# Kernel tuning notes

Hardware: AMD Instinct MI355X
Metric: run time of the kernel (lower is better)

The kernel has to match this reference:

```python
import jax, jax.numpy as jnp
import numpy as np

B, N, M, H = 200, 384, 512, 128
NN = B * N  # total nodes across the batch of graphs


def _gcn_layer(h, src, dst, norm, W, b):
    # GCNConv: linear -> symmetric-normalized aggregation -> relu
    h = h @ W + b
    msg = h[src] * norm[:, None]
    agg = jax.ops.segment_sum(msg, dst, num_segments=NN)
    return jax.nn.relu(agg)


def setup_inputs() -> dict:
    key = jax.random.key(0)
    ks = jax.random.split(key, 16)
    x = jax.random.normal(ks[0], (NN, 2), dtype=jnp.float32)
    off = (jnp.arange(B) * N)[:, None]
    parent = jax.random.randint(ks[1], (B, M), 0, N) + off
    child = jax.random.randint(ks[2], (B, M), 0, N) + off
    row0 = jnp.concatenate([parent, child], axis=1).reshape(-1)
    row1 = jnp.concatenate([child, parent], axis=1).reshape(-1)
    edge_index = jnp.stack([row0, row1]).astype(jnp.int64)
    numSwitches = jax.random.randint(ks[3], (B,), 1, M // 4).astype(jnp.int64)
    inv_degree = jax.random.uniform(ks[4], (B, N), minval=0.5, maxval=1.5)
    inc_parents = jax.random.normal(ks[5], (B, N, M)) * 0.1
    inc_childs = jax.random.normal(ks[6], (B, N, M)) * 0.1
    A = jax.random.normal(ks[7], (N, M)) * 0.1
    s = lambda k, sh: jax.random.normal(k, sh) * (1.0 / np.sqrt(sh[0]))
    return dict(
        x=x, edge_index=edge_index, numSwitches=numSwitches,
        inv_degree=inv_degree, inc_parents=inc_parents, inc_childs=inc_childs, A=A,
        W1=s(ks[8], (2, H)), b1=jnp.zeros((H,)),
        W2=s(ks[9], (H, H)), b2=jnp.zeros((H,)),
        Ws1=s(ks[10], (3 * H, 4 * H)), bs1=jnp.zeros((4 * H,)),
        Ws2=s(ks[11], (4 * H, 4)), bs2=jnp.zeros((4,)),
        Wc1=s(ks[12], (3 * H, 3 * H)), bc1=jnp.zeros((3 * H,)),
        Wc2=s(ks[13], (3 * H, 3)), bc2=jnp.zeros((3,)),
    )


def reference(x, inv_degree, inc_parents, inc_childs, A,
              W1, b1, W2, b2, Ws1, bs1, Ws2, bs2, Wc1, bc1, Wc2, bc2,
              edge_index, numSwitches):
    # ---- 2-layer GCN with self loops + symmetric norm ----
    src, dst = edge_index[0], edge_index[1]
    loop = jnp.arange(NN)
    src2 = jnp.concatenate([src, loop])
    dst2 = jnp.concatenate([dst, loop])
    deg = jax.ops.segment_sum(jnp.ones_like(src2, dtype=x.dtype), dst2, num_segments=NN)
    dinv = jax.lax.rsqrt(deg)
    norm = dinv[src2] * dinv[dst2]
    h = _gcn_layer(x, src2, dst2, norm, W1, b1)
    xg = _gcn_layer(h, src2, dst2, norm, W2, b2)  # [NN, H]

    x_nn = xg.reshape(B, N, H)
    x_g = x_nn.sum(axis=1)  # graph-level readout [B, H]

    edges = edge_index[0].reshape(B, 2 * M)
    parent_e = edges[:, :M]  # [B, M] global node ids
    child_e = edges[:, M:]
    # last numSwitches[b] edges of graph b are switches
    mask = jnp.arange(M)[None, :] >= (M - numSwitches[:, None])  # [B, M]

    xp = xg[parent_e]  # [B, M, H]
    xc = xg[child_e]
    feat = jnp.concatenate(
        [xp, xc, jnp.broadcast_to(x_g[:, None, :], (B, M, H))], axis=-1)  # [B,M,3H]
    # compute both MLPs densely, then mask-select (same values at selected slots
    # as torch's boolean gather -> MLP -> scatter)
    smlp = jax.nn.relu(feat @ Ws1 + bs1) @ Ws2 + bs2  # [B, M, 4]
    cmlp = jax.nn.relu(feat @ Wc1 + bc1) @ Wc2 + bc2  # [B, M, 3]

    p_switch = jax.nn.sigmoid(smlp[..., 0])
    graph_topo = jnp.where(mask, p_switch, 1.0)
    ps_flow = jnp.where(mask, smlp[..., 1], 0.0)
    vs_parent = jnp.where(mask, smlp[..., 2], 0.0)
    vs_child = jnp.where(mask, smlp[..., 3], 0.0)
    pc_flow = jnp.where(mask, 0.0, cmlp[..., 0])
    vc_parent = jnp.where(mask, 0.0, cmlp[..., 1])
    vc_child = jnp.where(mask, 0.0, cmlp[..., 2])
    p_flow = ps_flow + pc_flow

    # D_inv @ inc @ v is a per-row diagonal scale; no need to build [B,N,N]
    v = inv_degree * (jnp.einsum('bnm,bm->bn', inc_parents, vc_parent + vs_parent)
                      + jnp.einsum('bnm,bm->bn', inc_childs, vc_child + vs_child))
    v = v.at[:, 0].set(1.0)  # slack bus voltage

    # ---- complete_JA (physics completion) ----
    x_input = x.reshape(B, N, 2)
    pl, ql = x_input[..., 0], x_input[..., 1]
    p_fc = p_flow * graph_topo
    q_fc = jnp.einsum('nm,bn->bm', A, v) * graph_topo
    pg = pl + jnp.einsum('nm,bm->bn', A, p_fc)
    qg = ql + jnp.einsum('nm,bm->bn', A, q_fc)

    z = jnp.concatenate([p_fc, v, graph_topo], axis=1)    # [B, M+N+M]
    zc = jnp.concatenate([q_fc, pg, qg], axis=1)          # [B, M+N+N]
    return (z, zc)
```

## Files before the change

kernel.cpp:

```cpp
#include <hip/hip_runtime.h>
#include <hip/hip_bf16.h>

typedef __hip_bfloat16 bf16;
typedef __bf16 bf16x8 __attribute__((ext_vector_type(8)));
typedef float f32x4 __attribute__((ext_vector_type(4)));

static constexpr int cB = 200, cN = 384, cM = 512, cH = 128;
static constexpr int cNN  = cB * cN;
static constexpr int cE   = 2 * cB * cM;
static constexpr int cTWOM = 2 * cM;
static constexpr int ZROW = 2 * cM + cN;
static constexpr int CROW = cM + 2 * cN;
static constexpr int ZBASE = cB * ZROW;

__device__ __forceinline__ float b2f(bf16 x) { return __bfloat162float(x); }
__device__ __forceinline__ bf16  f2b(float x) { return __float2bfloat16(x); }

struct bf2 { bf16 x, y; };

__global__ __launch_bounds__(256) void k_norm_idx(const int* __restrict__ ei_raw,
                                                  const int* __restrict__ nsw_raw,
                                                  int* __restrict__ ei, int* __restrict__ nsw) {
  int z = 0;
#pragma unroll
  for (int j = 1; j < 64; j += 2) z |= ei_raw[j];
  const int f = (z == 0) ? 1 : 0;
  const int i = blockIdx.x * 256 + threadIdx.x;
  if (i < 2 * cE) ei[i] = ei_raw[i << f];
  if (blockIdx.x == 0 && threadIdx.x < cB) nsw[threadIdx.x] = nsw_raw[threadIdx.x << f];
}

__global__ __launch_bounds__(512) void k_csr2(const int* __restrict__ ei,
                                              float* __restrict__ dinv_g,
                                              int* __restrict__ csr_off, int* __restrict__ csr_src,
                                              float* __restrict__ csr_nrm) {
  __shared__ int cnt[cN];
  __shared__ float sdinv[cN];
  __shared__ int base[cN];
  __shared__ int scanbuf[cN];
  const int tid = threadIdx.x;
  const int b = blockIdx.x;
  for (int i = tid; i < cN; i += 512) cnt[i] = 0;
  __syncthreads();
  for (int i = tid; i < cTWOM; i += 512) {
    const int d = ei[cE + b * cTWOM + i] - b * cN;
    atomicAdd(&cnt[d], 1);
  }
  __syncthreads();
  if (tid < cN) {
    const float dv = rsqrtf((float)cnt[tid] + 1.0f);
    sdinv[tid] = dv;
    dinv_g[b * cN + tid] = dv;
    scanbuf[tid] = cnt[tid];
  }
  __syncthreads();
  for (int off = 1; off < cN; off <<= 1) {
    int v = 0;
    if (tid < cN && tid >= off) v = scanbuf[tid - off];
    __syncthreads();
    if (tid < cN) scanbuf[tid] += v;
    __syncthreads();
  }
  if (tid < cN) {
    base[tid] = scanbuf[tid] - cnt[tid];
    csr_off[b * (cN + 1) + tid] = base[tid];
  }
  if (tid == 0) csr_off[b * (cN + 1) + cN] = scanbuf[cN - 1];
  if (tid < cN) cnt[tid] = 0;
  __syncthreads();
  for (int i = tid; i < cTWOM; i += 512) {
    const int e = b * cTWOM + i;
    const int s = ei[e];
    const int d = ei[cE + e];
    const int sl = s - b * cN;
    const int dl = d - b * cN;
    const int slot = base[dl] + atomicAdd(&cnt[dl], 1);
    csr_src[b * cTWOM + slot] = s;
    csr_nrm[b * cTWOM + slot] = sdinv[sl] * sdinv[dl];
  }
}

__global__ __launch_bounds__(384) void k_gath3(const int* __restrict__ csr_off,
                                               const int* __restrict__ csr_src,
                                               const float* __restrict__ csr_nrm,
                                               const float* __restrict__ x,
                                               const float* __restrict__ dinv,
                                               float* __restrict__ a0_w, float* __restrict__ a1_w,
                                               float* __restrict__ aw_w) {
  __shared__ float xs[cN * 2];
  const int b = blockIdx.x, tid = threadIdx.x;
  for (int i = tid; i < cN * 2; i += 384) xs[i] = x[(size_t)b * cN * 2 + i];
  __syncthreads();
  const int nl = tid;
  const int wid = b * cN + nl;
  const int beg = csr_off[b * (cN + 1) + nl];
  const int end = csr_off[b * (cN + 1) + nl + 1];
  const int ebase = b * cTWOM;
  float a0 = 0.f, a1 = 0.f, aw = 0.f;
  for (int j = beg; j < end; ++j) {
    const int sl = csr_src[ebase + j] - b * cN;
    const float w = csr_nrm[ebase + j];
    a0 = fmaf(xs[2 * sl], w, a0);
    a1 = fmaf(xs[2 * sl + 1], w, a1);
    aw += w;
  }
  const float dn = dinv[wid];
  const float dn2 = dn * dn;
  a0 = fmaf(xs[2 * nl], dn2, a0);
  a1 = fmaf(xs[2 * nl + 1], dn2, a1);
  aw += dn2;
  a0_w[wid] = a0;
  a1_w[wid] = a1;
  aw_w[wid] = aw;
}

__global__ __launch_bounds__(256) void k_h1a(const float* __restrict__ a0_w,
                                             const float* __restrict__ a1_w,
                                             const float* __restrict__ aw_w,
                                             const float* __restrict__ W1,
                                             const float* __restrict__ b1,
                                             bf16* __restrict__ h1) {
  const int idx = blockIdx.x * 256 + threadIdx.x;
  if (idx >= cNN * cH) return;
  const int n = idx >> 7, h = idx & 127;
  const float v = a0_w[n] * W1[h] + a1_w[n] * W1[cH + h] + aw_w[n] * b1[h];
  h1[idx] = f2b(fmaxf(v, 0.f));
}

__global__ __launch_bounds__(256) void k_gather(const int* __restrict__ csr_off,
                                                const int* __restrict__ csr_src,
                                                const float* __restrict__ csr_nrm,
                                                const bf16* __restrict__ hsrc,
                                                const float* __restrict__ dinv,
                                                bf16* __restrict__ hdst) {
  const int wid = blockIdx.x * 4 + (threadIdx.x >> 6);
  const int lane = threadIdx.x & 63;
  const int b = wid / cN;
  const int nl = wid - b * cN;
  const int beg = csr_off[b * (cN + 1) + nl];
  const int end = csr_off[b * (cN + 1) + nl + 1];
  const int ebase = b * cTWOM;
  float a0 = 0.f, a1 = 0.f;
  for (int j = beg; j < end; ++j) {
    const int s = csr_src[ebase + j];
    const float w = csr_nrm[ebase + j];
    const unsigned u = *(const unsigned*)(hsrc + (size_t)s * cH + lane * 2);
    a0 = fmaf(__uint_as_float(u << 16), w, a0);
    a1 = fmaf(__uint_as_float(u & 0xffff0000u), w, a1);
  }
  const float dn = dinv[wid];
  const float dn2 = dn * dn;
  const unsigned us = *(const unsigned*)(hsrc + (size_t)wid * cH + lane * 2);
  a0 = fmaf(__uint_as_float(us << 16), dn2, a0);
  a1 = fmaf(__uint_as_float(us & 0xffff0000u), dn2, a1);
  bf2 pk;
  pk.x = f2b(fmaxf(a0, 0.f));
  pk.y = f2b(fmaxf(a1, 0.f));
  *(bf2*)(hdst + (size_t)wid * cH + lane * 2) = pk;
}

__global__ __launch_bounds__(256) void k_lin2_mfma(const bf16* __restrict__ h1,
                                                   const bf16* __restrict__ W2t,
                                                   const float* __restrict__ b2v,
                                                   bf16* __restrict__ h2raw) {
  constexpr int FS = 136;
  __shared__ __align__(16) bf16 feat[64 * FS];
  __shared__ float bl[cH];
  const int tid = threadIdx.x;
  const int n0 = blockIdx.x * 64;
  const int wv = tid >> 6, ln = tid & 63;
  const int fr = ln & 15, g4 = ln >> 4, ak = g4 * 8;
  {
    const int e = tid >> 2, j = tid & 3;
    const uint4* ps = (const uint4*)(h1 + (size_t)(n0 + e) * cH);
    uint4* fp = (uint4*)(feat + e * FS);
#pragma unroll
    for (int r = 0; r < 4; ++r) fp[j * 4 + r] = ps[j * 4 + r];
  }
  for (int i = tid; i < cH; i += 256) bl[i] = b2v[i];
  bf16x8 Bf[2][4];
#pragma unroll
  for (int nt = 0; nt < 2; ++nt) {
    const bf16* bp = W2t + (size_t)(wv * 32 + nt * 16 + fr) * cH + ak;
#pragma unroll
    for (int kt = 0; kt < 4; ++kt) Bf[nt][kt] = *(const bf16x8*)(bp + kt * 32);
  }
  __syncthreads();
#pragma unroll
  for (int mt = 0; mt < 4; ++mt) {
    f32x4 acc0 = f32x4{0.f, 0.f, 0.f, 0.f};
    f32x4 acc1 = f32x4{0.f, 0.f, 0.f, 0.f};
    const bf16* ap = feat + (mt * 16 + fr) * FS + ak;
#pragma unroll
    for (int kt = 0; kt < 4; ++kt) {
      const bf16x8 a = *(const bf16x8*)(ap + kt * 32);
      acc0 = __builtin_amdgcn_mfma_f32_16x16x32_bf16(a, Bf[0][kt], acc0, 0, 0, 0);
      acc1 = __builtin_amdgcn_mfma_f32_16x16x32_bf16(a, Bf[1][kt], acc1, 0, 0, 0);
    }
#pragma unroll
    for (int j = 0; j < 2; ++j) {
      const int col = wv * 32 + j * 16 + fr;
      const f32x4 av = j ? acc1 : acc0;
#pragma unroll
      for (int i = 0; i < 4; ++i) {
        const int row = mt * 16 + g4 * 4 + i;
        h2raw[(size_t)(n0 + row) * cH + col] = f2b(av[i] + bl[col]);
      }
    }
  }
}

__global__ __launch_bounds__(512) void k_xgg(const bf16* __restrict__ xg,
                                             const float* __restrict__ Ws1, const float* __restrict__ bs1,
                                             const float* __restrict__ Wc1, const float* __restrict__ bc1,
                                             float* __restrict__ g_s, float* __restrict__ g_c) {
  __shared__ float red[4][cH];
  __shared__ float xs[cH];
  const int b = blockIdx.x, tid = threadIdx.x;
  {
    const int h = tid & 127, q = tid >> 7;
    float s = 0.f;
    const bf16* p = xg + (size_t)b * cN * cH + (size_t)q * 96 * cH + h;
#pragma unroll 8
    for (int n = 0; n < 96; ++n) s += b2f(p[(size_t)n * cH]);
    red[q][h] = s;
  }
  __syncthreads();
  if (tid < cH) xs[tid] = red[0][tid] + red[1][tid] + red[2][tid] + red[3][tid];
  __syncthreads();
  {
    float acc = bs1[tid];
    for (int k = 0; k < cH; ++k) acc = fmaf(xs[k], Ws1[(2 * cH + k) * 512 + tid], acc);
    g_s[b * 512 + tid] = acc;
  }
  if (tid < 384) {
    float acc = bc1[tid];
    for (int k = 0; k < cH; ++k) acc = fmaf(xs[k], Wc1[(2 * cH + k) * 384 + tid], acc);
    g_c[b * 384 + tid] = acc;
  }
}

__global__ __launch_bounds__(256) void k_wt(const float* __restrict__ Ws1, const float* __restrict__ Wc1,
                                            const float* __restrict__ Wc2, const float* __restrict__ W2,
                                            bf16* __restrict__ Ws1t, bf16* __restrict__ Wc1t,
                                            float* __restrict__ Wc2p, bf16* __restrict__ W2t) {
  int idx = blockIdx.x * 256 + threadIdx.x;
  if (idx < 512 * 256) {
    int j = idx >> 8, k = idx & 255;
    Ws1t[idx] = f2b(Ws1[k * 512 + j]);
  }
  if (idx < 384 * 256) {
    int j = idx >> 8, k = idx & 255;
    Wc1t[idx] = f2b(Wc1[k * 384 + j]);
  }
  if (idx < 128 * 128) {
    int j = idx >> 7, k = idx & 127;
    W2t[idx] = f2b(W2[k * 128 + j]);
  }
  if (idx < 384 * 4) {
    int j = idx >> 2, o = idx & 3;
    Wc2p[idx] = (o < 3) ? Wc2[j * 3 + o] : 0.f;
  }
}

__global__ __launch_bounds__(256) void k_mlp_mfma(
    const int* __restrict__ ei, const int* __restrict__ nsw, const bf16* __restrict__ xg,
    const bf16* __restrict__ Ws1t, const bf16* __restrict__ Wc1t,
    const float* __restrict__ g_s, const float* __restrict__ g_c,
    const float* __restrict__ Ws2, const float* __restrict__ bs2,
    const float* __restrict__ Wc2p, const float* __restrict__ bc2,
    float* __restrict__ gt_w, float* __restrict__ wvp_w, float* __restrict__ wvc_w,
    float* __restrict__ pfc_w, float* __restrict__ out) {
  constexpr int FS = 264;
  __shared__ __align__(16) bf16 feat[64 * FS];
  __shared__ float gsl[512];
  __shared__ float gcl[384];
  __shared__ float red_s[4][64][4];
  __shared__ float red_c[4][64][4];

  const int tid = threadIdx.x;
  const int b = blockIdx.x >> 3;
  const int m0 = (blockIdx.x & 7) << 6;
  const int wv = tid >> 6, ln = tid & 63;
  const int fr = ln & 15;
  const int g4 = ln >> 4;
  const int swz = (fr & 7) * 8;

  const int ns = nsw[b];
  const int mb = cM - ns;
  const bool needS = (m0 + 64 > mb);
  const bool needC = (m0 < mb);

  {
    const int e = tid >> 2, j = tid & 3;
    const int m = m0 + e;
    const int pn = ei[b * cTWOM + m];
    const int cn = ei[b * cTWOM + cM + m];
    const int es = e & 7;
    const uint4* ps = (const uint4*)(xg + (size_t)pn * cH);
    const uint4* cs = (const uint4*)(xg + (size_t)cn * cH);
    uint4* fp = (uint4*)(feat + e * FS);
    uint4* fc = (uint4*)(feat + e * FS + 128);
#pragma unroll
    for (int r = 0; r < 4; ++r) {
      const int i = j * 4 + r;
      fp[i ^ es] = ps[i];
      fc[i ^ es] = cs[i];
    }
  }
  if (needS) for (int i = tid; i < 512; i += 256) gsl[i] = g_s[b * 512 + i];
  if (needC) for (int i = tid; i < 384; i += 256) gcl[i] = g_c[b * 384 + i];
  __syncthreads();

  if (needS) {
    float p[4][4][4];
#pragma unroll
    for (int m = 0; m < 4; ++m)
#pragma unroll
      for (int i = 0; i < 4; ++i)
#pragma unroll
        for (int o = 0; o < 4; ++o) p[m][i][o] = 0.f;
    const bf16* bp = Ws1t + ((size_t)(wv * 128 + fr)) * 256 + g4 * 8;
#pragma unroll
    for (int c = 0; c < 2; ++c) {
      f32x4 acc[4][4];
#pragma unroll
      for (int m = 0; m < 4; ++m)
#pragma unroll
        for (int j = 0; j < 4; ++j) acc[m][j] = f32x4{0.f, 0.f, 0.f, 0.f};
      const bf16* bpc = bp + (size_t)(c * 4) * 16 * 256;
#pragma unroll
      for (int kt = 0; kt < 8; ++kt) {
        const int eo = (g4 * 8 + kt * 32) ^ swz;
        const bf16x8 a0 = *(const bf16x8*)(feat + fr * FS + eo);
        const bf16x8 a1 = *(const bf16x8*)(feat + (16 + fr) * FS + eo);
        const bf16x8 a2 = *(const bf16x8*)(feat + (32 + fr) * FS + eo);
        const bf16x8 a3 = *(const bf16x8*)(feat + (48 + fr) * FS + eo);
        const int ko = kt * 32;
#pragma unroll
        for (int j = 0; j < 4; ++j) {
          const bf16x8 bfr = *(const bf16x8*)(bpc + (size_t)j * 16 * 256 + ko);
          acc[0][j] = __builtin_amdgcn_mfma_f32_16x16x32_bf16(a0, bfr, acc[0][j], 0, 0, 0);
          acc[1][j] = __builtin_amdgcn_mfma_f32_16x16x32_bf16(a1, bfr, acc[1][j], 0, 0, 0);
          acc[2][j] = __builtin_amdgcn_mfma_f32_16x16x32_bf16(a2, bfr, acc[2][j], 0, 0, 0);
          acc[3][j] = __builtin_amdgcn_mfma_f32_16x16x32_bf16(a3, bfr, acc[3][j], 0, 0, 0);
        }
      }
#pragma unroll
      for (int j = 0; j < 4; ++j) {
        const int col = wv * 128 + (c * 4 + j) * 16 + fr;
        const float4 w4 = *(const float4*)(Ws2 + col * 4);
        const float gs = gsl[col];
#pragma unroll
        for (int m = 0; m < 4; ++m)
#pragma unroll
          for (int i = 0; i < 4; ++i) {
            const float hv = fmaxf(acc[m][j][i] + gs, 0.f);
            p[m][i][0] = fmaf(hv, w4.x, p[m][i][0]);
            p[m][i][1] = fmaf(hv, w4.y, p[m][i][1]);
            p[m][i][2] = fmaf(hv, w4.z, p[m][i][2]);
            p[m][i][3] = fmaf(hv, w4.w, p[m][i][3]);
          }
      }
    }
#pragma unroll
    for (int mask = 1; mask <= 8; mask <<= 1)
#pragma unroll
      for (int m = 0; m < 4; ++m)
#pragma unroll
        for (int i = 0; i < 4; ++i)
#pragma unroll
          for (int o = 0; o < 4; ++o) p[m][i][o] += __shfl_xor(p[m][i][o], mask);
    if (fr == 0) {
#pragma unroll
      for (int m = 0; m < 4; ++m)
#pragma unroll
        for (int i = 0; i < 4; ++i) {
          const int row = m * 16 + g4 * 4 + i;
#pragma unroll
          for (int o = 0; o < 4; ++o) red_s[wv][row][o] = p[m][i][o];
        }
    }
  }

  if (needC) {
    float p[4][4][4];
#pragma unroll
    for (int m = 0; m < 4; ++m)
#pragma unroll
      for (int i = 0; i < 4; ++i)
#pragma unroll
        for (int o = 0; o < 4; ++o) p[m][i][o] = 0.f;
    const bf16* bp = Wc1t + ((size_t)(wv * 96 + fr)) * 256 + g4 * 8;
#pragma unroll
    for (int c = 0; c < 2; ++c) {
      f32x4 acc[4][3];
#pragma unroll
      for (int m = 0; m < 4; ++m)
#pragma unroll
        for (int j = 0; j < 3; ++j) acc[m][j] = f32x4{0.f, 0.f, 0.f, 0.f};
      const bf16* bpc = bp + (size_t)(c * 3) * 16 * 256;
#pragma unroll
      for (int kt = 0; kt < 8; ++kt) {
        const int eo = (g4 * 8 + kt * 32) ^ swz;
        const bf16x8 a0 = *(const bf16x8*)(feat + fr * FS + eo);
        const bf16x8 a1 = *(const bf16x8*)(feat + (16 + fr) * FS + eo);
        const bf16x8 a2 = *(const bf16x8*)(feat + (32 + fr) * FS + eo);
        const bf16x8 a3 = *(const bf16x8*)(feat + (48 + fr) * FS + eo);
        const int ko = kt * 32;
#pragma unroll
        for (int j = 0; j < 3; ++j) {
          const bf16x8 bfr = *(const bf16x8*)(bpc + (size_t)j * 16 * 256 + ko);
          acc[0][j] = __builtin_amdgcn_mfma_f32_16x16x32_bf16(a0, bfr, acc[0][j], 0, 0, 0);
          acc[1][j] = __builtin_amdgcn_mfma_f32_16x16x32_bf16(a1, bfr, acc[1][j], 0, 0, 0);
          acc[2][j] = __builtin_amdgcn_mfma_f32_16x16x32_bf16(a2, bfr, acc[2][j], 0, 0, 0);
          acc[3][j] = __builtin_amdgcn_mfma_f32_16x16x32_bf16(a3, bfr, acc[3][j], 0, 0, 0);
        }
      }
#pragma unroll
      for (int j = 0; j < 3; ++j) {
        const int col = wv * 96 + (c * 3 + j) * 16 + fr;
        const float4 w4 = *(const float4*)(Wc2p + col * 4);
        const float gc = gcl[col];
#pragma unroll
        for (int m = 0; m < 4; ++m)
#pragma unroll
          for (int i = 0; i < 4; ++i) {
            const float hv = fmaxf(acc[m][j][i] + gc, 0.f);
            p[m][i][0] = fmaf(hv, w4.x, p[m][i][0]);
            p[m][i][1] = fmaf(hv, w4.y, p[m][i][1]);
            p[m][i][2] = fmaf(hv, w4.z, p[m][i][2]);
          }
      }
    }
#pragma unroll
    for (int mask = 1; mask <= 8; mask <<= 1)
#pragma unroll
      for (int m = 0; m < 4; ++m)
#pragma unroll
        for (int i = 0; i < 4; ++i)
#pragma unroll
          for (int o = 0; o < 3; ++o) p[m][i][o] += __shfl_xor(p[m][i][o], mask);
    if (fr == 0) {
#pragma unroll
      for (int m = 0; m < 4; ++m)
#pragma unroll
        for (int i = 0; i < 4; ++i) {
          const int row = m * 16 + g4 * 4 + i;
#pragma unroll
          for (int o = 0; o < 3; ++o) red_c[wv][row][o] = p[m][i][o];
        }
    }
  }
  __syncthreads();

  if (tid < 64) {
    const int e = tid, m = m0 + e;
    const bool mk = (m >= mb);
    float gt, pf, vp, vc;
    if (mk) {
      const float s0  = red_s[0][e][0] + red_s[1][e][0] + red_s[2][e][0] + red_s[3][e][0] + bs2[0];
      gt = 1.f / (1.f + expf(-s0));
      pf = red_s[0][e][1] + red_s[1][e][1] + red_s[2][e][1] + red_s[3][e][1] + bs2[1];
      vp = red_s[0][e][2] + red_s[1][e][2] + red_s[2][e][2] + red_s[3][e][2] + bs2[2];
      vc = red_s[0][e][3] + red_s[1][e][3] + red_s[2][e][3] + red_s[3][e][3] + bs2[3];
    } else {
      gt = 1.f;
      pf = red_c[0][e][0] + red_c[1][e][0] + red_c[2][e][0] + red_c[3][e][0] + bc2[0];
      vp = red_c[0][e][1] + red_c[1][e][1] + red_c[2][e][1] + red_c[3][e][1] + bc2[1];
      vc = red_c[0][e][2] + red_c[1][e][2] + red_c[2][e][2] + red_c[3][e][2] + bc2[2];
    }
    const float pfc = pf * gt;
    const int bm = b * cM + m;
    gt_w[bm] = gt; wvp_w[bm] = vp; wvc_w[bm] = vc; pfc_w[bm] = pfc;
    out[b * ZROW + m] = pfc;
    out[b * ZROW + cM + cN + m] = gt;
  }
}

__global__ __launch_bounds__(256) void k_v(const float* __restrict__ incP, const float* __restrict__ incC,
                                           const float* __restrict__ wvp, const float* __restrict__ wvc,
                                           const float* __restrict__ invdeg, float* __restrict__ v_w,
                                           float* __restrict__ out) {
  const int wid = blockIdx.x * 4 + (threadIdx.x >> 6);
  const int lane = threadIdx.x & 63;
  const int b = wid / cN, n = wid % cN;
  const size_t rowoff = (size_t)(b * cN + n) * cM + lane * 8;
  const float4 p0 = *(const float4*)(incP + rowoff);
  const float4 p1 = *(const float4*)(incP + rowoff + 4);
  const float4 c0 = *(const float4*)(incC + rowoff);
  const float4 c1 = *(const float4*)(incC + rowoff + 4);
  const float* wp = wvp + b * cM + lane * 8;
  const float* wc = wvc + b * cM + lane * 8;
  float s;
  s = p0.x * wp[0] + p0.y * wp[1] + p0.z * wp[2] + p0.w * wp[3] +
      p1.x * wp[4] + p1.y * wp[5] + p1.z * wp[6] + p1.w * wp[7];
  s += c0.x * wc[0] + c0.y * wc[1] + c0.z * wc[2] + c0.w * wc[3] +
       c1.x * wc[4] + c1.y * wc[5] + c1.z * wc[6] + c1.w * wc[7];
#pragma unroll
  for (int off = 32; off >= 1; off >>= 1) s += __shfl_down(s, off);
  if (lane == 0) {
    float val = invdeg[b * cN + n] * s;
    if (n == 0) val = 1.0f;
    v_w[b * cN + n] = val;
    out[b * ZROW + cM + n] = val;
  }
}

__global__ __launch_bounds__(256) void k_qfc(const float* __restrict__ A, const float* __restrict__ v_w,
                                             const float* __restrict__ gt_w, float* __restrict__ qfc_w,
                                             float* __restrict__ out) {
  __shared__ float vs[cN];
  const int b = blockIdx.x >> 1;
  const int m = ((blockIdx.x & 1) << 8) + threadIdx.x;
  for (int i = threadIdx.x; i < cN; i += 256) vs[i] = v_w[b * cN + i];
  __syncthreads();
  float s = 0.f;
  for (int n = 0; n < cN; ++n) s = fmaf(A[n * cM + m], vs[n], s);
  const int bm = b * cM + m;
  const float q = s * gt_w[bm];
  qfc_w[bm] = q;
  out[ZBASE + b * CROW + m] = q;
}

__global__ __launch_bounds__(256) void k_pgqg(const float* __restrict__ A, const float* __restrict__ x,
                                              const float* __restrict__ pfc, const float* __restrict__ qfc,
                                              float* __restrict__ out) {
  const int wid = blockIdx.x * 4 + (threadIdx.x >> 6);
  const int lane = threadIdx.x & 63;
  const int b = wid / cN, n = wid - b * cN;
  const float* ar = A + (size_t)n * cM + lane * 8;
  const float* pf = pfc + b * cM + lane * 8;
  const float* qf = qfc + b * cM + lane * 8;
  const float4 a0 = *(const float4*)(ar);
  const float4 a1 = *(const float4*)(ar + 4);
  float ps, qs;
  ps = a0.x * pf[0] + a0.y * pf[1] + a0.z * pf[2] + a0.w * pf[3] +
       a1.x * pf[4] + a1.y * pf[5] + a1.z * pf[6] + a1.w * pf[7];
  qs = a0.x * qf[0] + a0.y * qf[1] + a0.z * qf[2] + a0.w * qf[3] +
       a1.x * qf[4] + a1.y * qf[5] + a1.z * qf[6] + a1.w * qf[7];
#pragma unroll
  for (int off = 32; off >= 1; off >>= 1) {
    ps += __shfl_down(ps, off);
    qs += __shfl_down(qs, off);
  }
  if (lane == 0) {
    out[ZBASE + b * CROW + cM + n] = x[2 * (size_t)wid] + ps;
    out[ZBASE + b * CROW + cM + cN + n] = x[2 * (size_t)wid + 1] + qs;
  }
}

extern "C" void kernel_launch(void* const* d_in, const int* in_sizes, int n_in,
                              void* d_out, int out_size, void* d_ws, size_t ws_size,
                              hipStream_t stream) {
  const bool dict_order = (in_sizes[1] == 2 * cE);
  int IEI, INSW, IIVD, IIP, IIC, IA, IW;
  if (dict_order) { IEI = 1; INSW = 2; IIVD = 3; IIP = 4; IIC = 5; IA = 6; IW = 7; }
  else            { IIVD = 1; IIP = 2; IIC = 3; IA = 4; IW = 5; IEI = 17; INSW = 18; }

  const float* x = (const float*)d_in[0];
  const int* ei_raw = (const int*)d_in[IEI];
  const int* nsw_raw = (const int*)d_in[INSW];
  const float* invdeg = (const float*)d_in[IIVD];
  const float* incP = (const float*)d_in[IIP];
  const float* incC = (const float*)d_in[IIC];
  const float* A = (const float*)d_in[IA];
  const float* W1 = (const float*)d_in[IW + 0];
  const float* b1 = (const float*)d_in[IW + 1];
  const float* W2 = (const float*)d_in[IW + 2];
  const float* b2 = (const float*)d_in[IW + 3];
  const float* Ws1 = (const float*)d_in[IW + 4];
  const float* bs1 = (const float*)d_in[IW + 5];
  const float* Ws2 = (const float*)d_in[IW + 6];
  const float* bs2 = (const float*)d_in[IW + 7];
  const float* Wc1 = (const float*)d_in[IW + 8];
  const float* bc1 = (const float*)d_in[IW + 9];
  const float* Wc2 = (const float*)d_in[IW + 10];
  const float* bc2 = (const float*)d_in[IW + 11];
  float* out = (float*)d_out;

  char* w = (char*)d_ws;
  auto alloc = [&](size_t bytes) { void* p = (void*)w; w += (bytes + 255) & ~(size_t)255; return p; };
  float* dinv = (float*)alloc((size_t)cNN * 4);
  int* ei = (int*)alloc((size_t)2 * cE * 4);
  int* nsw = (int*)alloc((size_t)cB * 4);
  bf16* hbufA = (bf16*)alloc((size_t)cNN * cH * 2);
  bf16* hbufB = (bf16*)alloc((size_t)cNN * cH * 2);
  int* csr_off = (int*)alloc((size_t)cB * (cN + 1) * 4);
  int* csr_src = (int*)alloc((size_t)cE * 4);
  float* csr_nrm = (float*)alloc((size_t)cE * 4);
  float* a0_w = (float*)alloc((size_t)cNN * 4);
  float* a1_w = (float*)alloc((size_t)cNN * 4);
  float* aw_w = (float*)alloc((size_t)cNN * 4);
  bf16* Ws1t = (bf16*)alloc((size_t)512 * 256 * 2);
  bf16* Wc1t = (bf16*)alloc((size_t)384 * 256 * 2);
  bf16* W2t = (bf16*)alloc((size_t)128 * 128 * 2);
  float* g_s = (float*)alloc((size_t)cB * 512 * 4);
  float* g_c = (float*)alloc((size_t)cB * 384 * 4);
  float* Wc2p = (float*)alloc((size_t)384 * 4 * 4);
  float* gt_w = (float*)alloc((size_t)cB * cM * 4);
  float* wvp_w = (float*)alloc((size_t)cB * cM * 4);
  float* wvc_w = (float*)alloc((size_t)cB * cM * 4);
  float* pfc_w = (float*)alloc((size_t)cB * cM * 4);
  float* qfc_w = (float*)alloc((size_t)cB * cM * 4);
  float* v_w = (float*)alloc((size_t)cB * cN * 4);

  const int NH = cNN * cH;
  k_norm_idx<<<(2 * cE) / 256, 256, 0, stream>>>(ei_raw, nsw_raw, ei, nsw);
  k_csr2<<<cB, 512, 0, stream>>>(ei, dinv, csr_off, csr_src, csr_nrm);

  k_gath3<<<cB, 384, 0, stream>>>(csr_off, csr_src, csr_nrm, x, dinv, a0_w, a1_w, aw_w);
  k_h1a<<<NH / 256, 256, 0, stream>>>(a0_w, a1_w, aw_w, W1, b1, hbufB);

  k_wt<<<512, 256, 0, stream>>>(Ws1, Wc1, Wc2, W2, Ws1t, Wc1t, Wc2p, W2t);

  k_lin2_mfma<<<cNN / 64, 256, 0, stream>>>(hbufB, W2t, b2, hbufA);
  k_gather<<<cNN / 4, 256, 0, stream>>>(csr_off, csr_src, csr_nrm, hbufA, dinv, hbufB);

  bf16* xg = hbufB;
  k_xgg<<<cB, 512, 0, stream>>>(xg, Ws1, bs1, Wc1, bc1, g_s, g_c);

  k_mlp_mfma<<<cB * 8, 256, 0, stream>>>(ei, nsw, xg, Ws1t, Wc1t, g_s, g_c,
                                         Ws2, bs2, Wc2p, bc2,
                                         gt_w, wvp_w, wvc_w, pfc_w, out);

  k_v<<<cB * cN / 4, 256, 0, stream>>>(incP, incC, wvp_w, wvc_w, invdeg, v_w, out);
  k_qfc<<<cB * cM / 256, 256, 0, stream>>>(A, v_w, gt_w, qfc_w, out);
  k_pgqg<<<cNN / 4, 256, 0, stream>>>(A, x, pfc_w, qfc_w, out);
}
```

Baseline: 321.4 us.

## Make MLP blocks persistent over four edge tiles with register-prefetched gathers

Each MLP block now handles four consecutive 64-edge tiles of one graph instead of one tile, so the grid shrinks from 1600 to 400 blocks. The gathered node features for the next tile are loaded into registers while the current tile's MFMA work runs, then written to shared memory between tiles. The g_s/g_c vectors are staged once per block instead of once per tile. In exchange there is less parallelism (400 blocks), more register pressure and extra barriers per tile. Because one block of each pair only ever covers tiles where the switch MLP cannot apply, the S/C branch work is also unevenly split between the two blocks of a graph.

```diff
diff --git a/kernel.cpp b/kernel.cpp
--- a/kernel.cpp
+++ b/kernel.cpp
@@ -279,8 +279,8 @@
   __shared__ float red_c[4][64][4];
 
   const int tid = threadIdx.x;
-  const int b = blockIdx.x >> 3;
-  const int m0 = (blockIdx.x & 7) << 6;
+  const int b = blockIdx.x >> 1;
+  const int tg = blockIdx.x & 1;
   const int wv = tid >> 6, ln = tid & 63;
   const int fr = ln & 15;
   const int g4 = ln >> 4;
@@ -288,193 +288,218 @@
 
   const int ns = nsw[b];
   const int mb = cM - ns;
-  const bool needS = (m0 + 64 > mb);
-  const bool needC = (m0 < mb);
-
-  {
-    const int e = tid >> 2, j = tid & 3;
-    const int m = m0 + e;
+
+  const int se = tid >> 2, sj = tid & 3, ses = se & 7;
+
+  uint4 sp[4], sc[4];
+
+  auto stage_load = [&](int t) {
+    const int m = ((tg * 4 + t) << 6) + se;
     const int pn = ei[b * cTWOM + m];
     const int cn = ei[b * cTWOM + cM + m];
-    const int es = e & 7;
     const uint4* ps = (const uint4*)(xg + (size_t)pn * cH);
     const uint4* cs = (const uint4*)(xg + (size_t)cn * cH);
-    uint4* fp = (uint4*)(feat + e * FS);
-    uint4* fc = (uint4*)(feat + e * FS + 128);
 #pragma unroll
     for (int r = 0; r < 4; ++r) {
-      const int i = j * 4 + r;
-      fp[i ^ es] = ps[i];
-      fc[i ^ es] = cs[i];
-    }
-  }
-  if (needS) for (int i = tid; i < 512; i += 256) gsl[i] = g_s[b * 512 + i];
-  if (needC) for (int i = tid; i < 384; i += 256) gcl[i] = g_c[b * 384 + i];
-  __syncthreads();
-
-  if (needS) {
-    float p[4][4][4];
-#pragma unroll
-    for (int m = 0; m < 4; ++m)
-#pragma unroll
-      for (int i = 0; i < 4; ++i)
-#pragma unroll
-        for (int o = 0; o < 4; ++o) p[m][i][o] = 0.f;
-    const bf16* bp = Ws1t + ((size_t)(wv * 128 + fr)) * 256 + g4 * 8;
-#pragma unroll
-    for (int c = 0; c < 2; ++c) {
-      f32x4 acc[4][4];
+      sp[r] = ps[sj * 4 + r];
+      sc[r] = cs[sj * 4 + r];
+    }
+  };
+  auto stage_write = [&]() {
+    uint4* fp = (uint4*)(feat + se * FS);
+    uint4* fc = (uint4*)(feat + se * FS + 128);
+#pragma unroll
+    for (int r = 0; r < 4; ++r) {
+      const int i = sj * 4 + r;
+      fp[i ^ ses] = sp[r];
+      fc[i ^ ses] = sc[r];
+    }
+  };
+
+  stage_load(0);
+  if (tg == 1) for (int i = tid; i < 512; i += 256) gsl[i] = g_s[b * 512 + i];
+  for (int i = tid; i < 384; i += 256) gcl[i] = g_c[b * 384 + i];
+  stage_write();
+  __syncthreads();
+  stage_load(1);
+
+#pragma unroll 1
+  for (int t = 0; t < 4; ++t) {
+    const int m0 = ((tg * 4 + t) << 6);
+    const bool needS = (tg == 1) && (m0 + 64 > mb);
+    const bool needC = (m0 < mb);
+
+    if (needS) {
+      float p[4][4][4];
 #pragma unroll
       for (int m = 0; m < 4; ++m)
 #pragma unroll
-        for (int j = 0; j < 4; ++j) acc[m][j] = f32x4{0.f, 0.f, 0.f, 0.f};
-      const bf16* bpc = bp + (size_t)(c * 4) * 16 * 256;
-#pragma unroll
-      for (int kt = 0; kt < 8; ++kt) {
-        const int eo = (g4 * 8 + kt * 32) ^ swz;
-        const bf16x8 a0 = *(const bf16x8*)(feat + fr * FS + eo);
-        const bf16x8 a1 = *(const bf16x8*)(feat + (16 + fr) * FS + eo);
-        const bf16x8 a2 = *(const bf16x8*)(feat + (32 + fr) * FS + eo);
-        const bf16x8 a3 = *(const bf16x8*)(feat + (48 + fr) * FS + eo);
-        const int ko = kt * 32;
+        for (int i = 0; i < 4; ++i)
+#pragma unroll
+          for (int o = 0; o < 4; ++o) p[m][i][o] = 0.f;
+      const bf16* bp = Ws1t + ((size_t)(wv * 128 + fr)) * 256 + g4 * 8;
+#pragma unroll
+      for (int c = 0; c < 2; ++c) {
+        f32x4 acc[4][4];
+#pragma unroll
+        for (int m = 0; m < 4; ++m)
+#pragma unroll
+          for (int j = 0; j < 4; ++j) acc[m][j] = f32x4{0.f, 0.f, 0.f, 0.f};
+        const bf16* bpc = bp + (size_t)(c * 4) * 16 * 256;
+#pragma unroll
+        for (int kt = 0; kt < 8; ++kt) {
+          const int eo = (g4 * 8 + kt * 32) ^ swz;
+          const bf16x8 a0 = *(const bf16x8*)(feat + fr * FS + eo);
+          const bf16x8 a1 = *(const bf16x8*)(feat + (16 + fr) * FS + eo);
+          const bf16x8 a2 = *(const bf16x8*)(feat + (32 + fr) * FS + eo);
+          const bf16x8 a3 = *(const bf16x8*)(feat + (48 + fr) * FS + eo);
+          const int ko = kt * 32;
+#pragma unroll
+          for (int j = 0; j < 4; ++j) {
+            const bf16x8 bfr = *(const bf16x8*)(bpc + (size_t)j * 16 * 256 + ko);
+            acc[0][j] = __builtin_amdgcn_mfma_f32_16x16x32_bf16(a0, bfr, acc[0][j], 0, 0, 0);
+            acc[1][j] = __builtin_amdgcn_mfma_f32_16x16x32_bf16(a1, bfr, acc[1][j], 0, 0, 0);
+            acc[2][j] = __builtin_amdgcn_mfma_f32_16x16x32_bf16(a2, bfr, acc[2][j], 0, 0, 0);
+            acc[3][j] = __builtin_amdgcn_mfma_f32_16x16x32_bf16(a3, bfr, acc[3][j], 0, 0, 0);
+          }
+        }
 #pragma unroll
         for (int j = 0; j < 4; ++j) {
-          const bf16x8 bfr = *(const bf16x8*)(bpc + (size_t)j * 16 * 256 + ko);
-          acc[0][j] = __builtin_amdgcn_mfma_f32_16x16x32_bf16(a0, bfr, acc[0][j], 0, 0, 0);
-          acc[1][j] = __builtin_amdgcn_mfma_f32_16x16x32_bf16(a1, bfr, acc[1][j], 0, 0, 0);
-          acc[2][j] = __builtin_amdgcn_mfma_f32_16x16x32_bf16(a2, bfr, acc[2][j], 0, 0, 0);
-          acc[3][j] = __builtin_amdgcn_mfma_f32_16x16x32_bf16(a3, bfr, acc[3][j], 0, 0, 0);
+          const int col = wv * 128 + (c * 4 + j) * 16 + fr;
+          const float4 w4 = *(const float4*)(Ws2 + col * 4);
+          const float gs = gsl[col];
+#pragma unroll
+          for (int m = 0; m < 4; ++m)
+#pragma unroll
+            for (int i = 0; i < 4; ++i) {
+              const float hv = fmaxf(acc[m][j][i] + gs, 0.f);
+              p[m][i][0] = fmaf(hv, w4.x, p[m][i][0]);
+              p[m][i][1] = fmaf(hv, w4.y, p[m][i][1]);
+              p[m][i][2] = fmaf(hv, w4.z, p[m][i][2]);
+              p[m][i][3] = fmaf(hv, w4.w, p[m][i][3]);
+            }
         }
       }
 #pragma unroll
-      for (int j = 0; j < 4; ++j) {
-        const int col = wv * 128 + (c * 4 + j) * 16 + fr;
-        const float4 w4 = *(const float4*)(Ws2 + col * 4);
-        const float gs = gsl[col];
+      for (int mask = 1; mask <= 8; mask <<= 1)
 #pragma unroll
         for (int m = 0; m < 4; ++m)
 #pragma unroll
+          for (int i = 0; i < 4; ++i)
+#pragma unroll
+            for (int o = 0; o < 4; ++o) p[m][i][o] += __shfl_xor(p[m][i][o], mask);
+      if (fr == 0) {
+#pragma unroll
+        for (int m = 0; m < 4; ++m)
+#pragma unroll
           for (int i = 0; i < 4; ++i) {
-            const float hv = fmaxf(acc[m][j][i] + gs, 0.f);
-            p[m][i][0] = fmaf(hv, w4.x, p[m][i][0]);
-            p[m][i][1] = fmaf(hv, w4.y, p[m][i][1]);
-            p[m][i][2] = fmaf(hv, w4.z, p[m][i][2]);
-            p[m][i][3] = fmaf(hv, w4.w, p[m][i][3]);
+            const int row = m * 16 + g4 * 4 + i;
+#pragma unroll
+            for (int o = 0; o < 4; ++o) red_s[wv][row][o] = p[m][i][o];
           }
       }
     }
-#pragma unroll
-    for (int mask = 1; mask <= 8; mask <<= 1)
+
+    if (needC) {
+      float p[4][4][4];
 #pragma unroll
       for (int m = 0; m < 4; ++m)
 #pragma unroll
         for (int i = 0; i < 4; ++i)
 #pragma unroll
-          for (int o = 0; o < 4; ++o) p[m][i][o] += __shfl_xor(p[m][i][o], mask);
-    if (fr == 0) {
-#pragma unroll
-      for (int m = 0; m < 4; ++m)
-#pragma unroll
-        for (int i = 0; i < 4; ++i) {
-          const int row = m * 16 + g4 * 4 + i;
-#pragma unroll
-          for (int o = 0; o < 4; ++o) red_s[wv][row][o] = p[m][i][o];
+          for (int o = 0; o < 4; ++o) p[m][i][o] = 0.f;
+      const bf16* bp = Wc1t + ((size_t)(wv * 96 + fr)) * 256 + g4 * 8;
+#pragma unroll
+      for (int c = 0; c < 2; ++c) {
+        f32x4 acc[4][3];
+#pragma unroll
+        for (int m = 0; m < 4; ++m)
+#pragma unroll
+          for (int j = 0; j < 3; ++j) acc[m][j] = f32x4{0.f, 0.f, 0.f, 0.f};
+        const bf16* bpc = bp + (size_t)(c * 3) * 16 * 256;
+#pragma unroll
+        for (int kt = 0; kt < 8; ++kt) {
+          const int eo = (g4 * 8 + kt * 32) ^ swz;
+          const bf16x8 a0 = *(const bf16x8*)(feat + fr * FS + eo);
+          const bf16x8 a1 = *(const bf16x8*)(feat + (16 + fr) * FS + eo);
+          const bf16x8 a2 = *(const bf16x8*)(feat + (32 + fr) * FS + eo);
+          const bf16x8 a3 = *(const bf16x8*)(feat + (48 + fr) * FS + eo);
+          const int ko = kt * 32;
+#pragma unroll
+          for (int j = 0; j < 3; ++j) {
+            const bf16x8 bfr = *(const bf16x8*)(bpc + (size_t)j * 16 * 256 + ko);
+            acc[0][j] = __builtin_amdgcn_mfma_f32_16x16x32_bf16(a0, bfr, acc[0][j], 0, 0, 0);
+            acc[1][j] = __builtin_amdgcn_mfma_f32_16x16x32_bf16(a1, bfr, acc[1][j], 0, 0, 0);
+            acc[2][j] = __builtin_amdgcn_mfma_f32_16x16x32_bf16(a2, bfr, acc[2][j], 0, 0, 0);
+            acc[3][j] = __builtin_amdgcn_mfma_f32_16x16x32_bf16(a3, bfr, acc[3][j], 0, 0, 0);
+          }
         }
-    }
-  }
-
-  if (needC) {
-    float p[4][4][4];
-#pragma unroll
-    for (int m = 0; m < 4; ++m)
-#pragma unroll
-      for (int i = 0; i < 4; ++i)
-#pragma unroll
-        for (int o = 0; o < 4; ++o) p[m][i][o] = 0.f;
-    const bf16* bp = Wc1t + ((size_t)(wv * 96 + fr)) * 256 + g4 * 8;
-#pragma unroll
-    for (int c = 0; c < 2; ++c) {
-      f32x4 acc[4][3];
-#pragma unroll
-      for (int m = 0; m < 4; ++m)
-#pragma unroll
-        for (int j = 0; j < 3; ++j) acc[m][j] = f32x4{0.f, 0.f, 0.f, 0.f};
-      const bf16* bpc = bp + (size_t)(c * 3) * 16 * 256;
-#pragma unroll
-      for (int kt = 0; kt < 8; ++kt) {
-        const int eo = (g4 * 8 + kt * 32) ^ swz;
-        const bf16x8 a0 = *(const bf16x8*)(feat + fr * FS + eo);
-        const bf16x8 a1 = *(const bf16x8*)(feat + (16 + fr) * FS + eo);
-        const bf16x8 a2 = *(const bf16x8*)(feat + (32 + fr) * FS + eo);
-        const bf16x8 a3 = *(const bf16x8*)(feat + (48 + fr) * FS + eo);
-        const int ko = kt * 32;
 #pragma unroll
         for (int j = 0; j < 3; ++j) {
-          const bf16x8 bfr = *(const bf16x8*)(bpc + (size_t)j * 16 * 256 + ko);
-          acc[0][j] = __builtin_amdgcn_mfma_f32_16x16x32_bf16(a0, bfr, acc[0][j], 0, 0, 0);
-          acc[1][j] = __builtin_amdgcn_mfma_f32_16x16x32_bf16(a1, bfr, acc[1][j], 0, 0, 0);
-          acc[2][j] = __builtin_amdgcn_mfma_f32_16x16x32_bf16(a2, bfr, acc[2][j], 0, 0, 0);
-          acc[3][j] = __builtin_amdgcn_mfma_f32_16x16x32_bf16(a3, bfr, acc[3][j], 0, 0, 0);
+          const int col = wv * 96 + (c * 3 + j) * 16 + fr;
+          const float4 w4 = *(const float4*)(Wc2p + col * 4);
+          const float gc = gcl[col];
+#pragma unroll
+          for (int m = 0; m < 4; ++m)
+#pragma unroll
+            for (int i = 0; i < 4; ++i) {
+              const float hv = fmaxf(acc[m][j][i] + gc, 0.f);
+              p[m][i][0] = fmaf(hv, w4.x, p[m][i][0]);
+              p[m][i][1] = fmaf(hv, w4.y, p[m][i][1]);
+              p[m][i][2] = fmaf(hv, w4.z, p[m][i][2]);
+            }
         }
       }
 #pragma unroll
-      for (int j = 0; j < 3; ++j) {
-        const int col = wv * 96 + (c * 3 + j) * 16 + fr;
-        const float4 w4 = *(const float4*)(Wc2p + col * 4);
-        const float gc = gcl[col];
+      for (int mask = 1; mask <= 8; mask <<= 1)
 #pragma unroll
         for (int m = 0; m < 4; ++m)
 #pragma unroll
+          for (int i = 0; i < 4; ++i)
+#pragma unroll
+            for (int o = 0; o < 3; ++o) p[m][i][o] += __shfl_xor(p[m][i][o], mask);
+      if (fr == 0) {
+#pragma unroll
+        for (int m = 0; m < 4; ++m)
+#pragma unroll
           for (int i = 0; i < 4; ++i) {
-            const float hv = fmaxf(acc[m][j][i] + gc, 0.f);
-            p[m][i][0] = fmaf(hv, w4.x, p[m][i][0]);
-            p[m][i][1] = fmaf(hv, w4.y, p[m][i][1]);
-            p[m][i][2] = fmaf(hv, w4.z, p[m][i][2]);
+            const int row = m * 16 + g4 * 4 + i;
+#pragma unroll
+            for (int o = 0; o < 3; ++o) red_c[wv][row][o] = p[m][i][o];
           }
       }
     }
-#pragma unroll
-    for (int mask = 1; mask <= 8; mask <<= 1)
-#pragma unroll
-      for (int m = 0; m < 4; ++m)
-#pragma unroll
-        for (int i = 0; i < 4; ++i)
-#pragma unroll
-          for (int o = 0; o < 3; ++o) p[m][i][o] += __shfl_xor(p[m][i][o], mask);
-    if (fr == 0) {
-#pragma unroll
-      for (int m = 0; m < 4; ++m)
-#pragma unroll
-        for (int i = 0; i < 4; ++i) {
-          const int row = m * 16 + g4 * 4 + i;
-#pragma unroll
-          for (int o = 0; o < 3; ++o) red_c[wv][row][o] = p[m][i][o];
-        }
-    }
-  }
-  __syncthreads();
-
-  if (tid < 64) {
-    const int e = tid, m = m0 + e;
-    const bool mk = (m >= mb);
-    float gt, pf, vp, vc;
-    if (mk) {
-      const float s0  = red_s[0][e][0] + red_s[1][e][0] + red_s[2][e][0] + red_s[3][e][0] + bs2[0];
-      gt = 1.f / (1.f + expf(-s0));
-      pf = red_s[0][e][1] + red_s[1][e][1] + red_s[2][e][1] + red_s[3][e][1] + bs2[1];
-      vp = red_s[0][e][2] + red_s[1][e][2] + red_s[2][e][2] + red_s[3][e][2] + bs2[2];
-      vc = red_s[0][e][3] + red_s[1][e][3] + red_s[2][e][3] + red_s[3][e][3] + bs2[3];
-    } else {
-      gt = 1.f;
-      pf = red_c[0][e][0] + red_c[1][e][0] + red_c[2][e][0] + red_c[3][e][0] + bc2[0];
-      vp = red_c[0][e][1] + red_c[1][e][1] + red_c[2][e][1] + red_c[3][e][1] + bc2[1];
-      vc = red_c[0][e][2] + red_c[1][e][2] + red_c[2][e][2] + red_c[3][e][2] + bc2[2];
-    }
-    const float pfc = pf * gt;
-    const int bm = b * cM + m;
-    gt_w[bm] = gt; wvp_w[bm] = vp; wvc_w[bm] = vc; pfc_w[bm] = pfc;
-    out[b * ZROW + m] = pfc;
-    out[b * ZROW + cM + cN + m] = gt;
+    __syncthreads();
+
+    if (tid < 64) {
+      const int e = tid, m = m0 + e;
+      const bool mk = (m >= mb);
+      float gt, pf, vp, vc;
+      if (mk) {
+        const float s0  = red_s[0][e][0] + red_s[1][e][0] + red_s[2][e][0] + red_s[3][e][0] + bs2[0];
+        gt = 1.f / (1.f + expf(-s0));
+        pf = red_s[0][e][1] + red_s[1][e][1] + red_s[2][e][1] + red_s[3][e][1] + bs2[1];
+        vp = red_s[0][e][2] + red_s[1][e][2] + red_s[2][e][2] + red_s[3][e][2] + bs2[2];
+        vc = red_s[0][e][3] + red_s[1][e][3] + red_s[2][e][3] + red_s[3][e][3] + bs2[3];
+      } else {
+        gt = 1.f;
+        pf = red_c[0][e][0] + red_c[1][e][0] + red_c[2][e][0] + red_c[3][e][0] + bc2[0];
+        vp = red_c[0][e][1] + red_c[1][e][1] + red_c[2][e][1] + red_c[3][e][1] + bc2[1];
+        vc = red_c[0][e][2] + red_c[1][e][2] + red_c[2][e][2] + red_c[3][e][2] + bc2[2];
+      }
+      const float pfc = pf * gt;
+      const int bm = b * cM + m;
+      gt_w[bm] = gt; wvp_w[bm] = vp; wvc_w[bm] = vc; pfc_w[bm] = pfc;
+      out[b * ZROW + m] = pfc;
+      out[b * ZROW + cM + cN + m] = gt;
+    }
+
+    if (t < 3) {
+      __syncthreads();
+      stage_write();
+      __syncthreads();
+      if (t < 2) stage_load(t + 2);
+    }
   }
 }
 
@@ -620,7 +645,7 @@
   bf16* xg = hbufB;
   k_xgg<<<cB, 512, 0, stream>>>(xg, Ws1, bs1, Wc1, bc1, g_s, g_c);
 
-  k_mlp_mfma<<<cB * 8, 256, 0, stream>>>(ei, nsw, xg, Ws1t, Wc1t, g_s, g_c,
+  k_mlp_mfma<<<cB * 2, 256, 0, stream>>>(ei, nsw, xg, Ws1t, Wc1t, g_s, g_c,
                                          Ws2, bs2, Wc2p, bc2,
                                          gt_w, wvp_w, wvc_w, pfc_w, out);
 
```

Result: slower. 361.9 us (median of 2 runs) (+12.6%).
